# Kernel tuning notes

Hardware: AMD Instinct MI355X
Metric: run time of the kernel (lower is better)

Reference implementation:

```python
import jax, jax.numpy as jnp
import numpy as np
from jax import lax

B, S, CIN, COUT = 32, 1024, 256, 256
EPS = 1e-5
LA = 0.1  # ResidualAttention la


def _cnorm(x, w, b):
    # ChannelNorm: mean/var over channel dim (axis=1); torch.var is unbiased (ddof=1)
    m = jnp.mean(x, axis=1, keepdims=True)
    v = jnp.var(x, axis=1, keepdims=True, ddof=1)
    return (x - m) * lax.rsqrt(v + EPS) * w[None, :, None] + b[None, :, None]


def _conv1d(x, w, pad):
    # x: [B, C_in, L], w: [C_out, C_in, K]
    return lax.conv_general_dilated(x, w, (1,), [(pad, pad)],
                                    dimension_numbers=('NCH', 'OIH', 'NCH'))


def _gate(x, fc_w):
    # ResidualAttention: 1x1 conv to 2 classes, mean + la*max over class dim, sigmoid
    y = _conv1d(x, fc_w, 0)                                   # [B, 2, L]
    score = jax.nn.sigmoid(jnp.mean(y, axis=1) + LA * jnp.max(y, axis=1))  # [B, L]
    return x * (1.0 + score[:, None, :])


def _pad_to(x, s):
    # pad_after_conv: zero-pad time dim back to s
    return jnp.pad(x, ((0, 0), (0, 0), (0, s - x.shape[-1])))


def _block(x, cn_w, cn_b, W, pad, fc_w, s):
    h = _conv1d(jax.nn.relu(_cnorm(x, cn_w, cn_b)), W, pad)
    return _pad_to(_gate(h, fc_w), s)


def setup_inputs() -> dict:
    key = jax.random.key(0)
    ks = jax.random.split(key, 8)
    d = {"inputs": jax.random.normal(ks[0], (B, S, CIN), jnp.float32)}
    cins = {4: CIN, 5: COUT, 6: COUT, 7: COUT, 8: COUT}
    for i, k in enumerate(range(4, 9)):
        cin = cins[k]
        d[f"cn{k}_w"] = jnp.ones((cin,), jnp.float32)
        d[f"cn{k}_b"] = jnp.zeros((cin,), jnp.float32)
        d[f"W{k}"] = jax.random.normal(ks[i + 1], (COUT, cin, k), jnp.float32) * (1.0 / np.sqrt(cin * k))
    d["fc_w"] = jax.random.normal(ks[6], (2, COUT, 1), jnp.float32) * (1.0 / np.sqrt(COUT))
    return d


def reference(inputs, cn4_w, cn4_b, W4, cn5_w, cn5_b, W5, cn6_w, cn6_b, W6,
              cn7_w, cn7_b, W7, cn8_w, cn8_b, W8, fc_w):
    x = jnp.transpose(inputs, (0, 2, 1))  # [B, C, S]
    s = x.shape[-1]
    # torch padding: int((k-1)/2) -> k=4:1, k=5:2, k=6:2, k=7:3, k=8:3
    x = _block(x, cn4_w, cn4_b, W4, 1, fc_w, s)
    x = _block(x, cn5_w, cn5_b, W5, 2, fc_w, s)
    x = _block(x, cn6_w, cn6_b, W6, 2, fc_w, s)
    x = _block(x, cn7_w, cn7_b, W7, 3, fc_w, s)
    x = _block(x, cn8_w, cn8_b, W8, 3, fc_w, s)
    return jnp.transpose(x, (0, 2, 1))  # [B, S, C_out]
```

## Files before the change

kernel.cpp:

```cpp
#include <hip/hip_runtime.h>
#include <hip/hip_bf16.h>

#define B_ 32
#define S_ 1024
#define C_ 256
#define SP 1040

typedef float f32x4 __attribute__((ext_vector_type(4)));
typedef __bf16 bf16x8 __attribute__((ext_vector_type(8)));

__global__ __launch_bounds__(256) void wcvt_kernel(const float* __restrict__ w,
                                                   __hip_bfloat16* __restrict__ wb,
                                                   int k, int n) {
    int i = blockIdx.x * 256 + threadIdx.x;
    if (i >= n) return;
    int e   = i & 7;
    int co  = (i >> 3) & 255;
    int g   = (i >> 11) & 3;
    int c32 = (i >> 13) & 7;
    int j   = i >> 16;
    int ci  = c32 * 32 + g * 8 + e;
    wb[i] = __float2bfloat16(w[(co * 256 + ci) * k + j]);
}

template<bool GATE, bool NORM>
__global__ __launch_bounds__(256) void prep_kernel(const float* __restrict__ in,
                                                   const float* __restrict__ fc,
                                                   const float* __restrict__ cw,
                                                   const float* __restrict__ cb,
                                                   __hip_bfloat16* __restrict__ yout,
                                                   float* __restrict__ fout) {
    const int lane = threadIdx.x & 63;
    const int rid  = blockIdx.x * 4 + (threadIdx.x >> 6);

    int b, t;
    __hip_bfloat16* drow = nullptr;
    if constexpr (NORM) {
        b = rid / SP;
        const int r = rid - b * SP;
        t = r - 8;
        drow = yout + ((size_t)(b * SP + r)) * C_ + lane * 4;
        if (t < 0 || t >= S_) {
            *(ushort4*)drow = make_ushort4(0, 0, 0, 0);
            return;
        }
    } else {
        b = rid >> 10;
        t = rid & 1023;
    }

    const float* row = in + ((size_t)(b * S_ + t)) * C_;
    f32x4 xv = *(const f32x4*)(row + lane * 4);

    if constexpr (GATE) {
        f32x4 f0 = *(const f32x4*)(fc + lane * 4);
        f32x4 f1 = *(const f32x4*)(fc + C_ + lane * 4);
        float p = xv.x * f0.x + xv.y * f0.y + xv.z * f0.z + xv.w * f0.w;
        float q = xv.x * f1.x + xv.y * f1.y + xv.z * f1.z + xv.w * f1.w;
#pragma unroll
        for (int m = 32; m >= 1; m >>= 1) {
            p += __shfl_xor(p, m, 64);
            q += __shfl_xor(q, m, 64);
        }
        float s = 0.5f * (p + q) + 0.1f * fmaxf(p, q);
        float score = 1.0f / (1.0f + expf(-s));
        float gmul = 1.0f + score;
        xv.x *= gmul; xv.y *= gmul; xv.z *= gmul; xv.w *= gmul;
    }

    if constexpr (NORM) {
        float s1 = xv.x + xv.y + xv.z + xv.w;
        float s2 = xv.x * xv.x + xv.y * xv.y + xv.z * xv.z + xv.w * xv.w;
#pragma unroll
        for (int m = 32; m >= 1; m >>= 1) {
            s1 += __shfl_xor(s1, m, 64);
            s2 += __shfl_xor(s2, m, 64);
        }
        float mean = s1 * (1.0f / 256.0f);
        float var  = fmaxf((s2 - 256.0f * mean * mean) * (1.0f / 255.0f), 0.0f);
        float inv  = rsqrtf(var + 1e-5f);
        f32x4 w4 = *(const f32x4*)(cw + lane * 4);
        f32x4 b4 = *(const f32x4*)(cb + lane * 4);
        float v0 = fmaxf(0.0f, (xv.x - mean) * inv * w4.x + b4.x);
        float v1 = fmaxf(0.0f, (xv.y - mean) * inv * w4.y + b4.y);
        float v2 = fmaxf(0.0f, (xv.z - mean) * inv * w4.z + b4.z);
        float v3 = fmaxf(0.0f, (xv.w - mean) * inv * w4.w + b4.w);
        union { ushort4 u; __hip_bfloat16 h[4]; } o;
        o.h[0] = __float2bfloat16(v0);
        o.h[1] = __float2bfloat16(v1);
        o.h[2] = __float2bfloat16(v2);
        o.h[3] = __float2bfloat16(v3);
        *(ushort4*)drow = o.u;
    } else {
        *(f32x4*)(fout + ((size_t)(b * S_ + t)) * C_ + lane * 4) = xv;
    }
}

template<int KS, int PAD, int LVALID>
__global__ __launch_bounds__(256) void conv_kernel(const __hip_bfloat16* __restrict__ y,
                                                   const __hip_bfloat16* __restrict__ wb,
                                                   float* __restrict__ h) {
    __shared__ alignas(16) __hip_bfloat16 ly[72 * 256];
    const int tid  = threadIdx.x;
    const int lane = tid & 63;
    const int wv   = tid >> 6;
    const int tt   = blockIdx.x & 15;
    const int b    = blockIdx.x >> 4;
    const int t0   = tt << 6;

    {
        const __hip_bfloat16* ybase = y + ((size_t)(b * SP + 8 + t0 - PAD)) * C_;
#pragma unroll
        for (int c = 0; c < 9; ++c) {
            int u = c * 256 + tid;
            int r = u >> 5, s = u & 31;
            bf16x8 v = *(const bf16x8*)(ybase + r * C_ + ((s ^ (r & 7)) << 3));
            *(bf16x8*)(ly + u * 8) = v;
        }
    }
    __syncthreads();

    f32x4 acc[4][4];
#pragma unroll
    for (int i = 0; i < 4; ++i)
#pragma unroll
        for (int j2 = 0; j2 < 4; ++j2)
            acc[i][j2] = f32x4{0.f, 0.f, 0.f, 0.f};

    const int l15 = lane & 15;
    const int g   = lane >> 4;
    const int co_base = wv * 64;

    for (int j = 0; j < KS; ++j) {
#pragma unroll
        for (int c32 = 0; c32 < 8; ++c32) {
            const __hip_bfloat16* wstep = wb + ((size_t)((j * 8 + c32) * 4 + g)) * 2048;
            bf16x8 a_f[4];
#pragma unroll
            for (int mf = 0; mf < 4; ++mf)
                a_f[mf] = *(const bf16x8*)(wstep + (co_base + mf * 16 + l15) * 8);
            bf16x8 b_f[4];
#pragma unroll
            for (int nf = 0; nf < 4; ++nf) {
                int r = nf * 16 + l15 + j;
                int ci8 = c32 * 4 + g;
                b_f[nf] = *(const bf16x8*)(ly + r * 256 + ((ci8 ^ (r & 7)) << 3));
            }
#pragma unroll
            for (int mf = 0; mf < 4; ++mf)
#pragma unroll
                for (int nf = 0; nf < 4; ++nf)
                    acc[mf][nf] = __builtin_amdgcn_mfma_f32_16x16x32_bf16(
                        a_f[mf], b_f[nf], acc[mf][nf], 0, 0, 0);
        }
    }

    float* hb = h + ((size_t)(b * S_ + t0)) * C_;
#pragma unroll
    for (int nf = 0; nf < 4; ++nf) {
        int tl = nf * 16 + l15;
#pragma unroll
        for (int mf = 0; mf < 4; ++mf) {
            int co = co_base + mf * 16 + g * 4;
            f32x4 v = acc[mf][nf];
            if (LVALID < S_ && (t0 + tl) >= LVALID)
                v = f32x4{0.f, 0.f, 0.f, 0.f};
            *(f32x4*)(hb + tl * 256 + co) = v;
        }
    }
}

extern "C" void kernel_launch(void* const* d_in, const int* in_sizes, int n_in,
                              void* d_out, int out_size, void* d_ws, size_t ws_size,
                              hipStream_t stream) {
    const float* inputs = (const float*)d_in[0];
    const float* cw[5] = { (const float*)d_in[1],  (const float*)d_in[4],
                           (const float*)d_in[7],  (const float*)d_in[10],
                           (const float*)d_in[13] };
    const float* cb[5] = { (const float*)d_in[2],  (const float*)d_in[5],
                           (const float*)d_in[8],  (const float*)d_in[11],
                           (const float*)d_in[14] };
    const float* Wf[5] = { (const float*)d_in[3],  (const float*)d_in[6],
                           (const float*)d_in[9],  (const float*)d_in[12],
                           (const float*)d_in[15] };
    const float* fc = (const float*)d_in[16];

    char* ws = (char*)d_ws;
    __hip_bfloat16* y = (__hip_bfloat16*)ws;
    float* h = (float*)(ws + 17039360);
    __hip_bfloat16* wb[5];
    size_t off = 17039360 + 33554432;
    for (int l = 0; l < 5; ++l) {
        wb[l] = (__hip_bfloat16*)(ws + off);
        off += (size_t)(l + 4) * 65536 * 2;
    }
    float* out = (float*)d_out;

    for (int l = 0; l < 5; ++l) {
        int k = l + 4, n = k * 65536;
        wcvt_kernel<<<(n + 255) / 256, 256, 0, stream>>>(Wf[l], wb[l], k, n);
    }

    const int GN = (B_ * SP) / 4;
    prep_kernel<false, true><<<GN, 256, 0, stream>>>(inputs, fc, cw[0], cb[0], y, nullptr);
    conv_kernel<4, 1, 1023><<<512, 256, 0, stream>>>(y, wb[0], h);
    prep_kernel<true, true><<<GN, 256, 0, stream>>>(h, fc, cw[1], cb[1], y, nullptr);
    conv_kernel<5, 2, 1024><<<512, 256, 0, stream>>>(y, wb[1], h);
    prep_kernel<true, true><<<GN, 256, 0, stream>>>(h, fc, cw[2], cb[2], y, nullptr);
    conv_kernel<6, 2, 1023><<<512, 256, 0, stream>>>(y, wb[2], h);
    prep_kernel<true, true><<<GN, 256, 0, stream>>>(h, fc, cw[3], cb[3], y, nullptr);
    conv_kernel<7, 3, 1024><<<512, 256, 0, stream>>>(y, wb[3], h);
    prep_kernel<true, true><<<GN, 256, 0, stream>>>(h, fc, cw[4], cb[4], y, nullptr);
    conv_kernel<8, 3, 1023><<<512, 256, 0, stream>>>(y, wb[4], h);
    prep_kernel<true, false><<<(B_ * S_) / 4, 256, 0, stream>>>(h, fc, nullptr, nullptr, nullptr, out);
}
```

Baseline: 379.5 us.

## Use 32x32x16 MFMA with two-batch blocks and bf16 intermediate activations

The conv kernel switches from 16x16x32 to 32x32x16 bf16 MFMA and reshapes the weight layout to match. Each 512-thread block now handles two batches so weight fragments are shared across more work. The conv output buffer is stored as bf16 instead of fp32, halving intermediate traffic to and from the prep kernels. The cost is extra rounding of pre-norm activations and gate inputs, which may reduce accuracy.

```diff
diff --git a/kernel.cpp b/kernel.cpp
--- a/kernel.cpp
+++ b/kernel.cpp
@@ -6,8 +6,10 @@
 #define C_ 256
 #define SP 1040
 
-typedef float f32x4 __attribute__((ext_vector_type(4)));
+typedef float f32x4  __attribute__((ext_vector_type(4)));
+typedef float f32x16 __attribute__((ext_vector_type(16)));
 typedef __bf16 bf16x8 __attribute__((ext_vector_type(8)));
+typedef __bf16 bf16x4 __attribute__((ext_vector_type(4)));
 
 __global__ __launch_bounds__(256) void wcvt_kernel(const float* __restrict__ w,
                                                    __hip_bfloat16* __restrict__ wb,
@@ -16,15 +18,16 @@
     if (i >= n) return;
     int e   = i & 7;
     int co  = (i >> 3) & 255;
-    int g   = (i >> 11) & 3;
+    int hh  = (i >> 11) & 1;
+    int ks  = (i >> 12) & 1;
     int c32 = (i >> 13) & 7;
     int j   = i >> 16;
-    int ci  = c32 * 32 + g * 8 + e;
+    int ci  = c32 * 32 + ks * 16 + hh * 8 + e;
     wb[i] = __float2bfloat16(w[(co * 256 + ci) * k + j]);
 }
 
-template<bool GATE, bool NORM>
-__global__ __launch_bounds__(256) void prep_kernel(const float* __restrict__ in,
+template<bool GATE, bool NORM, bool BF16IN>
+__global__ __launch_bounds__(256) void prep_kernel(const void* __restrict__ in_,
                                                    const float* __restrict__ fc,
                                                    const float* __restrict__ cw,
                                                    const float* __restrict__ cb,
@@ -49,8 +52,15 @@
         t = rid & 1023;
     }
 
-    const float* row = in + ((size_t)(b * S_ + t)) * C_;
-    f32x4 xv = *(const f32x4*)(row + lane * 4);
+    f32x4 xv;
+    if constexpr (BF16IN) {
+        const __hip_bfloat16* row = (const __hip_bfloat16*)in_ + ((size_t)(b * S_ + t)) * C_;
+        bf16x4 hv = *(const bf16x4*)(row + lane * 4);
+        xv.x = (float)hv[0]; xv.y = (float)hv[1]; xv.z = (float)hv[2]; xv.w = (float)hv[3];
+    } else {
+        const float* row = (const float*)in_ + ((size_t)(b * S_ + t)) * C_;
+        xv = *(const f32x4*)(row + lane * 4);
+    }
 
     if constexpr (GATE) {
         f32x4 f0 = *(const f32x4*)(fc + lane * 4);
@@ -85,11 +95,11 @@
         float v1 = fmaxf(0.0f, (xv.y - mean) * inv * w4.y + b4.y);
         float v2 = fmaxf(0.0f, (xv.z - mean) * inv * w4.z + b4.z);
         float v3 = fmaxf(0.0f, (xv.w - mean) * inv * w4.w + b4.w);
-        union { ushort4 u; __hip_bfloat16 h[4]; } o;
-        o.h[0] = __float2bfloat16(v0);
-        o.h[1] = __float2bfloat16(v1);
-        o.h[2] = __float2bfloat16(v2);
-        o.h[3] = __float2bfloat16(v3);
+        union { ushort4 u; __hip_bfloat16 e[4]; } o;
+        o.e[0] = __float2bfloat16(v0);
+        o.e[1] = __float2bfloat16(v1);
+        o.e[2] = __float2bfloat16(v2);
+        o.e[3] = __float2bfloat16(v3);
         *(ushort4*)drow = o.u;
     } else {
         *(f32x4*)(fout + ((size_t)(b * S_ + t)) * C_ + lane * 4) = xv;
@@ -97,75 +107,92 @@
 }
 
 template<int KS, int PAD, int LVALID>
-__global__ __launch_bounds__(256) void conv_kernel(const __hip_bfloat16* __restrict__ y,
+__global__ __launch_bounds__(512) void conv_kernel(const __hip_bfloat16* __restrict__ y,
                                                    const __hip_bfloat16* __restrict__ wb,
-                                                   float* __restrict__ h) {
-    __shared__ alignas(16) __hip_bfloat16 ly[72 * 256];
+                                                   __hip_bfloat16* __restrict__ hout) {
+    __shared__ alignas(16) __hip_bfloat16 ly[72 * 2 * 256];
     const int tid  = threadIdx.x;
     const int lane = tid & 63;
     const int wv   = tid >> 6;
     const int tt   = blockIdx.x & 15;
-    const int b    = blockIdx.x >> 4;
+    const int bp   = blockIdx.x >> 4;
     const int t0   = tt << 6;
-
-    {
-        const __hip_bfloat16* ybase = y + ((size_t)(b * SP + 8 + t0 - PAD)) * C_;
-#pragma unroll
-        for (int c = 0; c < 9; ++c) {
-            int u = c * 256 + tid;
-            int r = u >> 5, s = u & 31;
-            bf16x8 v = *(const bf16x8*)(ybase + r * C_ + ((s ^ (r & 7)) << 3));
-            *(bf16x8*)(ly + u * 8) = v;
-        }
+    const int b2   = bp * 2;
+
+#pragma unroll
+    for (int c = 0; c < 9; ++c) {
+        int u = c * 512 + tid;
+        int r = u >> 6, q = u & 63;
+        int bbs = q >> 5, s = q & 31;
+        const __hip_bfloat16* src = y + ((size_t)((b2 + bbs) * SP + 8 + t0 - PAD + r)) * C_
+                                      + ((s ^ (r & 7)) << 3);
+        *(bf16x8*)(ly + (size_t)u * 8) = *(const bf16x8*)src;
     }
     __syncthreads();
 
-    f32x4 acc[4][4];
-#pragma unroll
-    for (int i = 0; i < 4; ++i)
-#pragma unroll
-        for (int j2 = 0; j2 < 4; ++j2)
-            acc[i][j2] = f32x4{0.f, 0.f, 0.f, 0.f};
-
-    const int l15 = lane & 15;
-    const int g   = lane >> 4;
-    const int co_base = wv * 64;
-
-    for (int j = 0; j < KS; ++j) {
-#pragma unroll
-        for (int c32 = 0; c32 < 8; ++c32) {
-            const __hip_bfloat16* wstep = wb + ((size_t)((j * 8 + c32) * 4 + g)) * 2048;
-            bf16x8 a_f[4];
-#pragma unroll
-            for (int mf = 0; mf < 4; ++mf)
-                a_f[mf] = *(const bf16x8*)(wstep + (co_base + mf * 16 + l15) * 8);
-            bf16x8 b_f[4];
-#pragma unroll
-            for (int nf = 0; nf < 4; ++nf) {
-                int r = nf * 16 + l15 + j;
-                int ci8 = c32 * 4 + g;
-                b_f[nf] = *(const bf16x8*)(ly + r * 256 + ((ci8 ^ (r & 7)) << 3));
+    const int bb      = wv & 1;
+    const int co_base = (wv >> 1) * 64;
+    const int l31     = lane & 31;
+    const int hh      = lane >> 5;
+
+    f32x16 acc[2][2];
+#pragma unroll
+    for (int mf = 0; mf < 2; ++mf)
+#pragma unroll
+        for (int nf = 0; nf < 2; ++nf)
+#pragma unroll
+            for (int e = 0; e < 16; ++e)
+                acc[mf][nf][e] = 0.0f;
+
+    const __hip_bfloat16* abase = wb + (size_t)hh * 2048 + (size_t)(co_base + l31) * 8;
+    const __hip_bfloat16* lbb   = ly + bb * 256;
+
+#pragma unroll 4
+    for (int s = 0; s < KS * 8; ++s) {
+        const int j   = s >> 3;
+        const int c32 = s & 7;
+        bf16x8 a[2][2], bf[2][2];
+#pragma unroll
+        for (int ks = 0; ks < 2; ++ks)
+#pragma unroll
+            for (int mf = 0; mf < 2; ++mf)
+                a[ks][mf] = *(const bf16x8*)(abase + (size_t)(s * 4 + ks * 2) * 2048 + mf * 256);
+#pragma unroll
+        for (int ks = 0; ks < 2; ++ks)
+#pragma unroll
+            for (int nf = 0; nf < 2; ++nf) {
+                int r   = nf * 32 + l31 + j;
+                int ci8 = c32 * 4 + ks * 2 + hh;
+                bf[ks][nf] = *(const bf16x8*)(lbb + (size_t)r * 512 + ((ci8 ^ (r & 7)) << 3));
             }
 #pragma unroll
-            for (int mf = 0; mf < 4; ++mf)
-#pragma unroll
-                for (int nf = 0; nf < 4; ++nf)
-                    acc[mf][nf] = __builtin_amdgcn_mfma_f32_16x16x32_bf16(
-                        a_f[mf], b_f[nf], acc[mf][nf], 0, 0, 0);
-        }
-    }
-
-    float* hb = h + ((size_t)(b * S_ + t0)) * C_;
-#pragma unroll
-    for (int nf = 0; nf < 4; ++nf) {
-        int tl = nf * 16 + l15;
-#pragma unroll
-        for (int mf = 0; mf < 4; ++mf) {
-            int co = co_base + mf * 16 + g * 4;
-            f32x4 v = acc[mf][nf];
-            if (LVALID < S_ && (t0 + tl) >= LVALID)
-                v = f32x4{0.f, 0.f, 0.f, 0.f};
-            *(f32x4*)(hb + tl * 256 + co) = v;
+        for (int ks = 0; ks < 2; ++ks)
+#pragma unroll
+            for (int mf = 0; mf < 2; ++mf)
+#pragma unroll
+                for (int nf = 0; nf < 2; ++nf)
+                    acc[mf][nf] = __builtin_amdgcn_mfma_f32_32x32x16_bf16(
+                        a[ks][mf], bf[ks][nf], acc[mf][nf], 0, 0, 0);
+    }
+
+    __hip_bfloat16* hb = hout + ((size_t)((b2 + bb) * S_ + t0)) * C_ + co_base;
+#pragma unroll
+    for (int nf = 0; nf < 2; ++nf) {
+        int tl = nf * 32 + l31;
+        bool zout = (LVALID < S_) && (t0 + tl >= LVALID);
+#pragma unroll
+        for (int mf = 0; mf < 2; ++mf) {
+#pragma unroll
+            for (int r4 = 0; r4 < 4; ++r4) {
+                int co = mf * 32 + r4 * 8 + hh * 4;
+                union { ushort4 u; __hip_bfloat16 e[4]; } o;
+#pragma unroll
+                for (int q = 0; q < 4; ++q) {
+                    float v = zout ? 0.0f : acc[mf][nf][r4 * 4 + q];
+                    o.e[q] = __float2bfloat16(v);
+                }
+                *(ushort4*)(hb + (size_t)tl * C_ + co) = o.u;
+            }
         }
     }
 }
@@ -187,9 +214,9 @@
 
     char* ws = (char*)d_ws;
     __hip_bfloat16* y = (__hip_bfloat16*)ws;
-    float* h = (float*)(ws + 17039360);
+    __hip_bfloat16* h = (__hip_bfloat16*)(ws + 17039360);
     __hip_bfloat16* wb[5];
-    size_t off = 17039360 + 33554432;
+    size_t off = 17039360 + 16777216;
     for (int l = 0; l < 5; ++l) {
         wb[l] = (__hip_bfloat16*)(ws + off);
         off += (size_t)(l + 4) * 65536 * 2;
@@ -202,15 +229,15 @@
     }
 
     const int GN = (B_ * SP) / 4;
-    prep_kernel<false, true><<<GN, 256, 0, stream>>>(inputs, fc, cw[0], cb[0], y, nullptr);
-    conv_kernel<4, 1, 1023><<<512, 256, 0, stream>>>(y, wb[0], h);
-    prep_kernel<true, true><<<GN, 256, 0, stream>>>(h, fc, cw[1], cb[1], y, nullptr);
-    conv_kernel<5, 2, 1024><<<512, 256, 0, stream>>>(y, wb[1], h);
-    prep_kernel<true, true><<<GN, 256, 0, stream>>>(h, fc, cw[2], cb[2], y, nullptr);
-    conv_kernel<6, 2, 1023><<<512, 256, 0, stream>>>(y, wb[2], h);
-    prep_kernel<true, true><<<GN, 256, 0, stream>>>(h, fc, cw[3], cb[3], y, nullptr);
-    conv_kernel<7, 3, 1024><<<512, 256, 0, stream>>>(y, wb[3], h);
-    prep_kernel<true, true><<<GN, 256, 0, stream>>>(h, fc, cw[4], cb[4], y, nullptr);
-    conv_kernel<8, 3, 1023><<<512, 256, 0, stream>>>(y, wb[4], h);
-    prep_kernel<true, false><<<(B_ * S_) / 4, 256, 0, stream>>>(h, fc, nullptr, nullptr, nullptr, out);
-}
+    prep_kernel<false, true, false><<<GN, 256, 0, stream>>>(inputs, fc, cw[0], cb[0], y, nullptr);
+    conv_kernel<4, 1, 1023><<<256, 512, 0, stream>>>(y, wb[0], h);
+    prep_kernel<true, true, true><<<GN, 256, 0, stream>>>(h, fc, cw[1], cb[1], y, nullptr);
+    conv_kernel<5, 2, 1024><<<256, 512, 0, stream>>>(y, wb[1], h);
+    prep_kernel<true, true, true><<<GN, 256, 0, stream>>>(h, fc, cw[2], cb[2], y, nullptr);
+    conv_kernel<6, 2, 1023><<<256, 512, 0, stream>>>(y, wb[2], h);
+    prep_kernel<true, true, true><<<GN, 256, 0, stream>>>(h, fc, cw[3], cb[3], y, nullptr);
+    conv_kernel<7, 3, 1024><<<256, 512, 0, stream>>>(y, wb[3], h);
+    prep_kernel<true, true, true><<<GN, 256, 0, stream>>>(h, fc, cw[4], cb[4], y, nullptr);
+    conv_kernel<8, 3, 1023><<<256, 512, 0, stream>>>(y, wb[4], h);
+    prep_kernel<true, false, true><<<(B_ * S_) / 4, 256, 0, stream>>>(h, fc, nullptr, nullptr, nullptr, out);
+}
```

After: 374.7 us. No clear change (-1.3%).

## Fuse gate and channel-norm epilogue into conv kernel with 32x32 MFMA tiles

Applied to the files above, without the earlier changes.

The gate, channel norm, ReLU and bf16 conversion of the next layer move into the conv kernel's epilogue. This removes the fp32 intermediate h buffer and the separate prep passes between layers, and the kernel ping-pongs between two bf16 activation buffers. The conv tile grows to 128 timesteps using 32x32x16 MFMA with double-buffered fragment loads. The five weight conversions merge into one launch. Grid size falls from 512 to 256 blocks, which may underfill the GPU's CUs, and the cross-wave reductions add two block barriers.

```diff
diff --git a/kernel.cpp b/kernel.cpp
--- a/kernel.cpp
+++ b/kernel.cpp
@@ -6,168 +6,260 @@
 #define C_ 256
 #define SP 1040
 
-typedef float f32x4 __attribute__((ext_vector_type(4)));
+typedef float f32x4  __attribute__((ext_vector_type(4)));
+typedef float f32x16 __attribute__((ext_vector_type(16)));
 typedef __bf16 bf16x8 __attribute__((ext_vector_type(8)));
 
-__global__ __launch_bounds__(256) void wcvt_kernel(const float* __restrict__ w,
-                                                   __hip_bfloat16* __restrict__ wb,
-                                                   int k, int n) {
+__global__ __launch_bounds__(256) void wcvt_all(
+        const float* __restrict__ w4, const float* __restrict__ w5,
+        const float* __restrict__ w6, const float* __restrict__ w7,
+        const float* __restrict__ w8, __hip_bfloat16* __restrict__ wb) {
     int i = blockIdx.x * 256 + threadIdx.x;
-    if (i >= n) return;
-    int e   = i & 7;
-    int co  = (i >> 3) & 255;
-    int g   = (i >> 11) & 3;
-    int c32 = (i >> 13) & 7;
-    int j   = i >> 16;
-    int ci  = c32 * 32 + g * 8 + e;
-    wb[i] = __float2bfloat16(w[(co * 256 + ci) * k + j]);
-}
-
-template<bool GATE, bool NORM>
-__global__ __launch_bounds__(256) void prep_kernel(const float* __restrict__ in,
-                                                   const float* __restrict__ fc,
-                                                   const float* __restrict__ cw,
-                                                   const float* __restrict__ cb,
-                                                   __hip_bfloat16* __restrict__ yout,
-                                                   float* __restrict__ fout) {
+    const float* src; int base, k;
+    if      (i <  262144) { src = w4; base = 0;       k = 4; }
+    else if (i <  589824) { src = w5; base = 262144;  k = 5; }
+    else if (i <  983040) { src = w6; base = 589824;  k = 6; }
+    else if (i < 1441792) { src = w7; base = 983040;  k = 7; }
+    else                  { src = w8; base = 1441792; k = 8; }
+    int ii = i - base;
+    int e = ii & 7, co = (ii >> 3) & 255, hh = (ii >> 11) & 1;
+    int ks = (ii >> 12) & 1, c32 = (ii >> 13) & 7, j = ii >> 16;
+    int ci = c32 * 32 + ks * 16 + hh * 8 + e;
+    wb[i] = __float2bfloat16(src[(co * 256 + ci) * k + j]);
+}
+
+__global__ __launch_bounds__(256) void zeroh_kernel(__hip_bfloat16* __restrict__ y) {
+    int i = blockIdx.x * 256 + threadIdx.x;
+    int b = i >> 9, rr = (i >> 5) & 15, s = i & 31;
+    int row = (rr < 8) ? rr : (1024 + rr);
+    uint4 z = make_uint4(0, 0, 0, 0);
+    *(uint4*)(y + ((size_t)(b * SP + row)) * C_ + s * 8) = z;
+}
+
+__global__ __launch_bounds__(256) void prep0_kernel(const float* __restrict__ in,
+                                                    const float* __restrict__ cw,
+                                                    const float* __restrict__ cb,
+                                                    __hip_bfloat16* __restrict__ yout) {
     const int lane = threadIdx.x & 63;
-    const int rid  = blockIdx.x * 4 + (threadIdx.x >> 6);
-
-    int b, t;
-    __hip_bfloat16* drow = nullptr;
-    if constexpr (NORM) {
-        b = rid / SP;
-        const int r = rid - b * SP;
-        t = r - 8;
-        drow = yout + ((size_t)(b * SP + r)) * C_ + lane * 4;
-        if (t < 0 || t >= S_) {
-            *(ushort4*)drow = make_ushort4(0, 0, 0, 0);
-            return;
-        }
-    } else {
-        b = rid >> 10;
-        t = rid & 1023;
-    }
-
-    const float* row = in + ((size_t)(b * S_ + t)) * C_;
-    f32x4 xv = *(const f32x4*)(row + lane * 4);
-
-    if constexpr (GATE) {
-        f32x4 f0 = *(const f32x4*)(fc + lane * 4);
-        f32x4 f1 = *(const f32x4*)(fc + C_ + lane * 4);
-        float p = xv.x * f0.x + xv.y * f0.y + xv.z * f0.z + xv.w * f0.w;
-        float q = xv.x * f1.x + xv.y * f1.y + xv.z * f1.z + xv.w * f1.w;
-#pragma unroll
-        for (int m = 32; m >= 1; m >>= 1) {
-            p += __shfl_xor(p, m, 64);
-            q += __shfl_xor(q, m, 64);
-        }
-        float s = 0.5f * (p + q) + 0.1f * fmaxf(p, q);
-        float score = 1.0f / (1.0f + expf(-s));
-        float gmul = 1.0f + score;
-        xv.x *= gmul; xv.y *= gmul; xv.z *= gmul; xv.w *= gmul;
-    }
-
-    if constexpr (NORM) {
-        float s1 = xv.x + xv.y + xv.z + xv.w;
-        float s2 = xv.x * xv.x + xv.y * xv.y + xv.z * xv.z + xv.w * xv.w;
-#pragma unroll
-        for (int m = 32; m >= 1; m >>= 1) {
-            s1 += __shfl_xor(s1, m, 64);
-            s2 += __shfl_xor(s2, m, 64);
-        }
-        float mean = s1 * (1.0f / 256.0f);
-        float var  = fmaxf((s2 - 256.0f * mean * mean) * (1.0f / 255.0f), 0.0f);
-        float inv  = rsqrtf(var + 1e-5f);
-        f32x4 w4 = *(const f32x4*)(cw + lane * 4);
-        f32x4 b4 = *(const f32x4*)(cb + lane * 4);
-        float v0 = fmaxf(0.0f, (xv.x - mean) * inv * w4.x + b4.x);
-        float v1 = fmaxf(0.0f, (xv.y - mean) * inv * w4.y + b4.y);
-        float v2 = fmaxf(0.0f, (xv.z - mean) * inv * w4.z + b4.z);
-        float v3 = fmaxf(0.0f, (xv.w - mean) * inv * w4.w + b4.w);
-        union { ushort4 u; __hip_bfloat16 h[4]; } o;
-        o.h[0] = __float2bfloat16(v0);
-        o.h[1] = __float2bfloat16(v1);
-        o.h[2] = __float2bfloat16(v2);
-        o.h[3] = __float2bfloat16(v3);
-        *(ushort4*)drow = o.u;
-    } else {
-        *(f32x4*)(fout + ((size_t)(b * S_ + t)) * C_ + lane * 4) = xv;
-    }
-}
-
-template<int KS, int PAD, int LVALID>
-__global__ __launch_bounds__(256) void conv_kernel(const __hip_bfloat16* __restrict__ y,
-                                                   const __hip_bfloat16* __restrict__ wb,
-                                                   float* __restrict__ h) {
-    __shared__ alignas(16) __hip_bfloat16 ly[72 * 256];
+    const int sl   = lane & 31;
+    const int rid  = (blockIdx.x * 4 + (threadIdx.x >> 6)) * 2 + (lane >> 5);
+    const int b = rid / SP;
+    const int t = (rid - b * SP) - 8;
+    __hip_bfloat16* drow = yout + (size_t)rid * C_ + sl * 8;
+    if (t < 0 || t >= S_) { *(uint4*)drow = make_uint4(0, 0, 0, 0); return; }
+
+    const float* row = in + ((size_t)(b * S_ + t)) * C_ + sl * 8;
+    f32x4 x0 = *(const f32x4*)row;
+    f32x4 x1 = *(const f32x4*)(row + 4);
+    float s1 = x0.x + x0.y + x0.z + x0.w + x1.x + x1.y + x1.z + x1.w;
+    float s2 = x0.x*x0.x + x0.y*x0.y + x0.z*x0.z + x0.w*x0.w
+             + x1.x*x1.x + x1.y*x1.y + x1.z*x1.z + x1.w*x1.w;
+#pragma unroll
+    for (int m = 16; m >= 1; m >>= 1) {
+        s1 += __shfl_xor(s1, m, 64);
+        s2 += __shfl_xor(s2, m, 64);
+    }
+    float mean = s1 * (1.0f / 256.0f);
+    float var  = fmaxf((s2 - 256.0f * mean * mean) * (1.0f / 255.0f), 0.0f);
+    float inv  = rsqrtf(var + 1e-5f);
+    f32x4 w0 = *(const f32x4*)(cw + sl * 8);
+    f32x4 w1 = *(const f32x4*)(cw + sl * 8 + 4);
+    f32x4 b0 = *(const f32x4*)(cb + sl * 8);
+    f32x4 b1 = *(const f32x4*)(cb + sl * 8 + 4);
+    union { uint4 u; __hip_bfloat16 e[8]; } o;
+    o.e[0] = __float2bfloat16(fmaxf(0.f, (x0.x - mean)*inv*w0.x + b0.x));
+    o.e[1] = __float2bfloat16(fmaxf(0.f, (x0.y - mean)*inv*w0.y + b0.y));
+    o.e[2] = __float2bfloat16(fmaxf(0.f, (x0.z - mean)*inv*w0.z + b0.z));
+    o.e[3] = __float2bfloat16(fmaxf(0.f, (x0.w - mean)*inv*w0.w + b0.w));
+    o.e[4] = __float2bfloat16(fmaxf(0.f, (x1.x - mean)*inv*w1.x + b1.x));
+    o.e[5] = __float2bfloat16(fmaxf(0.f, (x1.y - mean)*inv*w1.y + b1.y));
+    o.e[6] = __float2bfloat16(fmaxf(0.f, (x1.z - mean)*inv*w1.z + b1.z));
+    o.e[7] = __float2bfloat16(fmaxf(0.f, (x1.w - mean)*inv*w1.w + b1.w));
+    *(uint4*)drow = o.u;
+}
+
+template<int KS, int PAD, int LVALID, bool LAST>
+__global__ __launch_bounds__(256, 2) void conv_fused(
+        const __hip_bfloat16* __restrict__ y,
+        const __hip_bfloat16* __restrict__ wb,
+        __hip_bfloat16* __restrict__ ynext,
+        float* __restrict__ fout,
+        const float* __restrict__ fc,
+        const float* __restrict__ cwn,
+        const float* __restrict__ cbn) {
+    __shared__ alignas(16) __hip_bfloat16 ly[135 * 256];
+    __shared__ float redpq[128][4];
+    __shared__ float redss[128][4];
     const int tid  = threadIdx.x;
     const int lane = tid & 63;
     const int wv   = tid >> 6;
-    const int tt   = blockIdx.x & 15;
-    const int b    = blockIdx.x >> 4;
-    const int t0   = tt << 6;
+    const int tt   = blockIdx.x & 7;
+    const int b    = blockIdx.x >> 3;
+    const int t0   = tt << 7;
 
     {
-        const __hip_bfloat16* ybase = y + ((size_t)(b * SP + 8 + t0 - PAD)) * C_;
-#pragma unroll
-        for (int c = 0; c < 9; ++c) {
+        const __hip_bfloat16* yb = y + ((size_t)(b * SP + 8 + t0 - PAD)) * C_;
+#pragma unroll
+        for (int c = 0; c < 17; ++c) {
             int u = c * 256 + tid;
-            int r = u >> 5, s = u & 31;
-            bf16x8 v = *(const bf16x8*)(ybase + r * C_ + ((s ^ (r & 7)) << 3));
-            *(bf16x8*)(ly + u * 8) = v;
+            if (u < 4320) {
+                int r = u >> 5, s2 = u & 31;
+                *(bf16x8*)(ly + (size_t)u * 8) =
+                    *(const bf16x8*)(yb + (size_t)r * C_ + ((s2 ^ (r & 7)) << 3));
+            }
         }
     }
     __syncthreads();
 
-    f32x4 acc[4][4];
-#pragma unroll
-    for (int i = 0; i < 4; ++i)
-#pragma unroll
-        for (int j2 = 0; j2 < 4; ++j2)
-            acc[i][j2] = f32x4{0.f, 0.f, 0.f, 0.f};
-
-    const int l15 = lane & 15;
-    const int g   = lane >> 4;
-    const int co_base = wv * 64;
-
-    for (int j = 0; j < KS; ++j) {
-#pragma unroll
-        for (int c32 = 0; c32 < 8; ++c32) {
-            const __hip_bfloat16* wstep = wb + ((size_t)((j * 8 + c32) * 4 + g)) * 2048;
-            bf16x8 a_f[4];
-#pragma unroll
-            for (int mf = 0; mf < 4; ++mf)
-                a_f[mf] = *(const bf16x8*)(wstep + (co_base + mf * 16 + l15) * 8);
-            bf16x8 b_f[4];
-#pragma unroll
-            for (int nf = 0; nf < 4; ++nf) {
-                int r = nf * 16 + l15 + j;
-                int ci8 = c32 * 4 + g;
-                b_f[nf] = *(const bf16x8*)(ly + r * 256 + ((ci8 ^ (r & 7)) << 3));
-            }
-#pragma unroll
-            for (int mf = 0; mf < 4; ++mf)
-#pragma unroll
-                for (int nf = 0; nf < 4; ++nf)
-                    acc[mf][nf] = __builtin_amdgcn_mfma_f32_16x16x32_bf16(
-                        a_f[mf], b_f[nf], acc[mf][nf], 0, 0, 0);
-        }
-    }
-
-    float* hb = h + ((size_t)(b * S_ + t0)) * C_;
-#pragma unroll
-    for (int nf = 0; nf < 4; ++nf) {
-        int tl = nf * 16 + l15;
-#pragma unroll
-        for (int mf = 0; mf < 4; ++mf) {
-            int co = co_base + mf * 16 + g * 4;
-            f32x4 v = acc[mf][nf];
-            if (LVALID < S_ && (t0 + tl) >= LVALID)
-                v = f32x4{0.f, 0.f, 0.f, 0.f};
-            *(f32x4*)(hb + tl * 256 + co) = v;
-        }
-    }
+    const int cog = wv & 1;
+    const int tq  = wv >> 1;
+    const int l31 = lane & 31;
+    const int hh  = lane >> 5;
+
+    f32x16 acc[4][2];
+#pragma unroll
+    for (int mf = 0; mf < 4; ++mf)
+#pragma unroll
+        for (int nf = 0; nf < 2; ++nf)
+#pragma unroll
+            for (int e = 0; e < 16; ++e)
+                acc[mf][nf][e] = 0.0f;
+
+    const __hip_bfloat16* abase = wb + (size_t)hh * 2048 + (size_t)(cog * 128 + l31) * 8;
+    const int rbase = tq * 64 + l31;
+
+    bf16x8 aF[2][2][4], bF[2][2][2];
+
+#define LOADS(ST, S) { \
+    const int jj_ = (S) >> 3, cc_ = (S) & 7; \
+    _Pragma("unroll") for (int ks = 0; ks < 2; ++ks) { \
+        _Pragma("unroll") for (int mf = 0; mf < 4; ++mf) \
+            aF[ST][ks][mf] = *(const bf16x8*)(abase + (size_t)((S) * 4 + ks * 2) * 2048 + mf * 256); \
+        _Pragma("unroll") for (int nf = 0; nf < 2; ++nf) { \
+            int r_ = rbase + nf * 32 + jj_; \
+            int ci8_ = cc_ * 4 + ks * 2 + hh; \
+            bF[ST][ks][nf] = *(const bf16x8*)(ly + (size_t)r_ * 256 + ((ci8_ ^ (r_ & 7)) << 3)); \
+        } } }
+
+#define MM(ST) { \
+    _Pragma("unroll") for (int ks = 0; ks < 2; ++ks) \
+    _Pragma("unroll") for (int mf = 0; mf < 4; ++mf) \
+    _Pragma("unroll") for (int nf = 0; nf < 2; ++nf) \
+        acc[mf][nf] = __builtin_amdgcn_mfma_f32_32x32x16_bf16( \
+            aF[ST][ks][mf], bF[ST][ks][nf], acc[mf][nf], 0, 0, 0); }
+
+    constexpr int NS = KS * 8;
+    LOADS(0, 0)
+#pragma unroll 1
+    for (int sb = 0; sb < NS / 2 - 1; ++sb) {
+        const int s0 = sb * 2;
+        LOADS(1, s0 + 1)
+        MM(0)
+        LOADS(0, s0 + 2)
+        MM(1)
+    }
+    LOADS(1, NS - 1)
+    MM(0)
+    MM(1)
+#undef LOADS
+#undef MM
+
+    const int tl0 = tq * 64 + l31, tl1 = tl0 + 32;
+
+    float p0 = 0.f, q0 = 0.f, p1 = 0.f, q1 = 0.f;
+#pragma unroll
+    for (int mf = 0; mf < 4; ++mf)
+#pragma unroll
+        for (int r4 = 0; r4 < 4; ++r4) {
+            int cb4 = cog * 128 + mf * 32 + r4 * 8 + hh * 4;
+            f32x4 f0 = *(const f32x4*)(fc + cb4);
+            f32x4 f1 = *(const f32x4*)(fc + 256 + cb4);
+#pragma unroll
+            for (int qd = 0; qd < 4; ++qd) {
+                float a0 = acc[mf][0][r4 * 4 + qd];
+                float a1 = acc[mf][1][r4 * 4 + qd];
+                p0 += f0[qd] * a0; q0 += f1[qd] * a0;
+                p1 += f0[qd] * a1; q1 += f1[qd] * a1;
+            }
+        }
+    p0 += __shfl_xor(p0, 32, 64); q0 += __shfl_xor(q0, 32, 64);
+    p1 += __shfl_xor(p1, 32, 64); q1 += __shfl_xor(q1, 32, 64);
+    if (!hh) {
+        redpq[tl0][cog * 2] = p0; redpq[tl0][cog * 2 + 1] = q0;
+        redpq[tl1][cog * 2] = p1; redpq[tl1][cog * 2 + 1] = q1;
+    }
+    __syncthreads();
+    float P0 = p0 + redpq[tl0][(1 - cog) * 2], Q0 = q0 + redpq[tl0][(1 - cog) * 2 + 1];
+    float P1 = p1 + redpq[tl1][(1 - cog) * 2], Q1 = q1 + redpq[tl1][(1 - cog) * 2 + 1];
+    float sc0 = 0.5f * (P0 + Q0) + 0.1f * fmaxf(P0, Q0);
+    float sc1 = 0.5f * (P1 + Q1) + 0.1f * fmaxf(P1, Q1);
+    float g0 = 1.0f + 1.0f / (1.0f + expf(-sc0));
+    float g1 = 1.0f + 1.0f / (1.0f + expf(-sc1));
+    const bool z0 = (LVALID < S_) && (t0 + tl0 >= LVALID);
+    const bool z1 = (LVALID < S_) && (t0 + tl1 >= LVALID);
+
+    if constexpr (LAST) {
+#pragma unroll
+        for (int mf = 0; mf < 4; ++mf)
+#pragma unroll
+            for (int r4 = 0; r4 < 4; ++r4) {
+                int cb4 = cog * 128 + mf * 32 + r4 * 8 + hh * 4;
+                f32x4 v0, v1;
+#pragma unroll
+                for (int qd = 0; qd < 4; ++qd) {
+                    v0[qd] = z0 ? 0.0f : acc[mf][0][r4 * 4 + qd] * g0;
+                    v1[qd] = z1 ? 0.0f : acc[mf][1][r4 * 4 + qd] * g1;
+                }
+                *(f32x4*)(fout + ((size_t)(b * S_ + t0 + tl0)) * C_ + cb4) = v0;
+                *(f32x4*)(fout + ((size_t)(b * S_ + t0 + tl1)) * C_ + cb4) = v1;
+            }
+        return;
+    }
+
+    float s10 = 0.f, s20 = 0.f, s11 = 0.f, s21 = 0.f;
+#pragma unroll
+    for (int mf = 0; mf < 4; ++mf)
+#pragma unroll
+        for (int e = 0; e < 16; ++e) {
+            float a0 = acc[mf][0][e] * g0; acc[mf][0][e] = a0; s10 += a0; s20 += a0 * a0;
+            float a1 = acc[mf][1][e] * g1; acc[mf][1][e] = a1; s11 += a1; s21 += a1 * a1;
+        }
+    s10 += __shfl_xor(s10, 32, 64); s20 += __shfl_xor(s20, 32, 64);
+    s11 += __shfl_xor(s11, 32, 64); s21 += __shfl_xor(s21, 32, 64);
+    if (!hh) {
+        redss[tl0][cog * 2] = s10; redss[tl0][cog * 2 + 1] = s20;
+        redss[tl1][cog * 2] = s11; redss[tl1][cog * 2 + 1] = s21;
+    }
+    __syncthreads();
+    float S10 = s10 + redss[tl0][(1 - cog) * 2], S20 = s20 + redss[tl0][(1 - cog) * 2 + 1];
+    float S11 = s11 + redss[tl1][(1 - cog) * 2], S21 = s21 + redss[tl1][(1 - cog) * 2 + 1];
+    float mean0 = S10 * (1.0f / 256.0f);
+    float inv0  = rsqrtf(fmaxf((S20 - 256.0f * mean0 * mean0) * (1.0f / 255.0f), 0.0f) + 1e-5f);
+    float mean1 = S11 * (1.0f / 256.0f);
+    float inv1  = rsqrtf(fmaxf((S21 - 256.0f * mean1 * mean1) * (1.0f / 255.0f), 0.0f) + 1e-5f);
+
+    __hip_bfloat16* yb0 = ynext + ((size_t)(b * SP + 8 + t0 + tl0)) * C_;
+    __hip_bfloat16* yb1 = ynext + ((size_t)(b * SP + 8 + t0 + tl1)) * C_;
+#pragma unroll
+    for (int mf = 0; mf < 4; ++mf)
+#pragma unroll
+        for (int r4 = 0; r4 < 4; ++r4) {
+            int cb4 = cog * 128 + mf * 32 + r4 * 8 + hh * 4;
+            f32x4 wv4 = *(const f32x4*)(cwn + cb4);
+            f32x4 bv4 = *(const f32x4*)(cbn + cb4);
+            union { ushort4 u; __hip_bfloat16 e[4]; } o0, o1;
+#pragma unroll
+            for (int qd = 0; qd < 4; ++qd) {
+                float v0 = z0 ? fmaxf(bv4[qd], 0.f)
+                              : fmaxf(0.f, (acc[mf][0][r4 * 4 + qd] - mean0) * inv0 * wv4[qd] + bv4[qd]);
+                float v1 = z1 ? fmaxf(bv4[qd], 0.f)
+                              : fmaxf(0.f, (acc[mf][1][r4 * 4 + qd] - mean1) * inv1 * wv4[qd] + bv4[qd]);
+                o0.e[qd] = __float2bfloat16(v0);
+                o1.e[qd] = __float2bfloat16(v1);
+            }
+            *(ushort4*)(yb0 + cb4) = o0.u;
+            *(ushort4*)(yb1 + cb4) = o1.u;
+        }
 }
 
 extern "C" void kernel_launch(void* const* d_in, const int* in_sizes, int n_in,
@@ -186,31 +278,18 @@
     const float* fc = (const float*)d_in[16];
 
     char* ws = (char*)d_ws;
-    __hip_bfloat16* y = (__hip_bfloat16*)ws;
-    float* h = (float*)(ws + 17039360);
-    __hip_bfloat16* wb[5];
-    size_t off = 17039360 + 33554432;
-    for (int l = 0; l < 5; ++l) {
-        wb[l] = (__hip_bfloat16*)(ws + off);
-        off += (size_t)(l + 4) * 65536 * 2;
-    }
+    __hip_bfloat16* yP = (__hip_bfloat16*)ws;
+    __hip_bfloat16* yQ = (__hip_bfloat16*)(ws + 17039360);
+    __hip_bfloat16* wb = (__hip_bfloat16*)(ws + 34078720);
     float* out = (float*)d_out;
 
-    for (int l = 0; l < 5; ++l) {
-        int k = l + 4, n = k * 65536;
-        wcvt_kernel<<<(n + 255) / 256, 256, 0, stream>>>(Wf[l], wb[l], k, n);
-    }
-
-    const int GN = (B_ * SP) / 4;
-    prep_kernel<false, true><<<GN, 256, 0, stream>>>(inputs, fc, cw[0], cb[0], y, nullptr);
-    conv_kernel<4, 1, 1023><<<512, 256, 0, stream>>>(y, wb[0], h);
-    prep_kernel<true, true><<<GN, 256, 0, stream>>>(h, fc, cw[1], cb[1], y, nullptr);
-    conv_kernel<5, 2, 1024><<<512, 256, 0, stream>>>(y, wb[1], h);
-    prep_kernel<true, true><<<GN, 256, 0, stream>>>(h, fc, cw[2], cb[2], y, nullptr);
-    conv_kernel<6, 2, 1023><<<512, 256, 0, stream>>>(y, wb[2], h);
-    prep_kernel<true, true><<<GN, 256, 0, stream>>>(h, fc, cw[3], cb[3], y, nullptr);
-    conv_kernel<7, 3, 1024><<<512, 256, 0, stream>>>(y, wb[3], h);
-    prep_kernel<true, true><<<GN, 256, 0, stream>>>(h, fc, cw[4], cb[4], y, nullptr);
-    conv_kernel<8, 3, 1023><<<512, 256, 0, stream>>>(y, wb[4], h);
-    prep_kernel<true, false><<<(B_ * S_) / 4, 256, 0, stream>>>(h, fc, nullptr, nullptr, nullptr, out);
-}
+    wcvt_all<<<7680, 256, 0, stream>>>(Wf[0], Wf[1], Wf[2], Wf[3], Wf[4], wb);
+    zeroh_kernel<<<64, 256, 0, stream>>>(yQ);
+    prep0_kernel<<<4160, 256, 0, stream>>>(inputs, cw[0], cb[0], yP);
+
+    conv_fused<4, 1, 1023, false><<<256, 256, 0, stream>>>(yP, wb,           yQ, nullptr, fc, cw[1], cb[1]);
+    conv_fused<5, 2, 1024, false><<<256, 256, 0, stream>>>(yQ, wb +  262144, yP, nullptr, fc, cw[2], cb[2]);
+    conv_fused<6, 2, 1023, false><<<256, 256, 0, stream>>>(yP, wb +  589824, yQ, nullptr, fc, cw[3], cb[3]);
+    conv_fused<7, 3, 1024, false><<<256, 256, 0, stream>>>(yQ, wb +  983040, yP, nullptr, fc, cw[4], cb[4]);
+    conv_fused<8, 3, 1023, true ><<<256, 256, 0, stream>>>(yP, wb + 1441792, nullptr, out, fc, nullptr, nullptr);
+}
```

Result: no change. 383.4 us (+1.0%).
